# Kernel tuning notes

Measured on AMD Instinct MI355X. Metric: run time of the kernel, lower is better.

The kernel has to match this reference:

```python
import jax, jax.numpy as jnp
import numpy as np

IN_DIM = 256
LN_EPS = 1e-05


def _xavier(key, shape):
    fan_in, fan_out = shape[1], shape[0]
    a = np.sqrt(6.0 / (fan_in + fan_out)).astype(np.float32)
    return jax.random.uniform(key, shape, jnp.float32, -a, a)


def setup_inputs() -> dict:
    key = jax.random.key(0)
    ks = jax.random.split(key, 4)
    B, C, H, W = 32, IN_DIM, 32, 32
    x = jax.random.normal(ks[0], (B, C, H, W), jnp.float32)
    y = jax.random.normal(ks[1], (B, C, H, W), jnp.float32)
    # nn.MultiheadAttention in_proj: rows [0:C] -> Wq, [C:2C] -> Wk (V/out_proj
    # never influence the returned attention weights, so omitted).
    Wq = _xavier(ks[2], (C, C))
    Wk = _xavier(ks[3], (C, C))
    bq = jnp.zeros((C,), jnp.float32)
    bk = jnp.zeros((C,), jnp.float32)
    # norm1 LayerNorm affine params (norm2 is unused in forward).
    gamma = jnp.ones((C,), jnp.float32)
    beta = jnp.zeros((C,), jnp.float32)
    return {"x": x, "y": y, "gamma": gamma, "beta": beta,
            "Wq": Wq, "Wk": Wk, "bq": bq, "bk": bk}


def _layernorm(t, gamma, beta):
    mu = jnp.mean(t, axis=-1, keepdims=True)
    var = jnp.mean(jnp.square(t - mu), axis=-1, keepdims=True)
    return (t - mu) * jax.lax.rsqrt(var + LN_EPS) * gamma + beta


def reference(x, y, gamma, beta, Wq, Wk, bq, bk):
    B, C = x.shape[0], x.shape[1]
    # [B,C,H,W] -> [B, N, C]
    xs = x.reshape(B, C, -1).transpose(0, 2, 1)
    ys = y.reshape(B, C, -1).transpose(0, 2, 1)
    q = _layernorm(xs, gamma, beta) @ Wq.T + bq   # [B,N,C]
    k = _layernorm(ys, gamma, beta) @ Wk.T + bk   # [B,N,C]
    scale = 1.0 / np.sqrt(C).astype(np.float32)   # single head: head_dim = C
    scores = jnp.einsum('bnc,bmc->bnm', q, k) * scale  # [B,N,N]
    w = jax.nn.softmax(scores, axis=-1)
    # module returns weight.diagonal(dim1=1, dim2=2) -> [B, N]
    return jnp.diagonal(w, axis1=1, axis2=2)
```

## Files before the change

### kernel.cpp

```cpp
#include <hip/hip_runtime.h>
#include <math.h>

#define BATCH 32
#define CDIM  256
#define NDIM  1024
#define BN    (BATCH * NDIM)
#define BNC   ((size_t)BATCH * NDIM * CDIM)
#define LN_EPSF 1e-5f
#define SCALE 0.0625f

typedef __attribute__((ext_vector_type(8))) __bf16 bf16x8;
typedef __attribute__((ext_vector_type(4))) float f32x4;
typedef __attribute__((ext_vector_type(4))) unsigned short ushort4v;

static __device__ __forceinline__ unsigned short f2bf(float f) {
  unsigned u = __float_as_uint(f);
  unsigned r = (u + 0x7FFFu + ((u >> 16) & 1u)) >> 16;
  return (unsigned short)r;
}
static __device__ __forceinline__ float bf2f(unsigned short h) {
  return __uint_as_float(((unsigned)h) << 16);
}
static __device__ __forceinline__ void gload16(const void* g, void* l) {
  __builtin_amdgcn_global_load_lds((const __attribute__((address_space(1))) void*)g,
                                   (__attribute__((address_space(3))) void*)l, 16, 0, 0);
}


__global__ __launch_bounds__(256) void wsplit_k(const float* __restrict__ Wq,
                                                const float* __restrict__ Wk,
                                                unsigned short* __restrict__ wp) {
  int idx = blockIdx.x * 256 + threadIdx.x;
  float vq = Wq[idx];
  unsigned short hq = f2bf(vq);
  wp[idx] = hq;
  wp[65536 + idx] = f2bf(vq - bf2f(hq));
  float vk = Wk[idx];
  unsigned short hk = f2bf(vk);
  wp[131072 + idx] = hk;
  wp[196608 + idx] = f2bf(vk - bf2f(hk));
}

__global__ __launch_bounds__(256) void proj_k(const float* __restrict__ x,
                                              const float* __restrict__ y,
                                              const float* __restrict__ gamma,
                                              const float* __restrict__ beta,
                                              const float* __restrict__ bq,
                                              const float* __restrict__ bk,
                                              const unsigned short* __restrict__ wp,
                                              unsigned short* __restrict__ planes) {
  __shared__ unsigned short Lh[64][264];
  __shared__ unsigned short Ll[64][264];
  __shared__ float psum[16][64], psq[16][64];
  __shared__ float mu[64], ri[64], gl[CDIM], bl[CDIM], bias_s[CDIM];

  const int t = threadIdx.x;
  const int bz = blockIdx.y;
  const int b = bz >> 1, which = bz & 1;
  const int n0 = blockIdx.x * 64;
  const float* src = which ? y : x;

  gl[t] = gamma[t];
  bl[t] = beta[t];
  bias_s[t] = (which ? bk : bq)[t];

  const int nq = (t & 15) * 4;
  const int cs = (t >> 4) * 16;
  float4 xr[16];
#pragma unroll
  for (int i = 0; i < 16; ++i)
    xr[i] = *(const float4*)(src + ((size_t)b * CDIM + cs + i) * NDIM + n0 + nq);

  {
    float s[4] = {0.f, 0.f, 0.f, 0.f}, q[4] = {0.f, 0.f, 0.f, 0.f};
#pragma unroll
    for (int i = 0; i < 16; ++i) {
      float v0 = xr[i].x, v1 = xr[i].y, v2 = xr[i].z, v3 = xr[i].w;
      s[0] += v0; q[0] += v0 * v0;
      s[1] += v1; q[1] += v1 * v1;
      s[2] += v2; q[2] += v2 * v2;
      s[3] += v3; q[3] += v3 * v3;
    }
#pragma unroll
    for (int j = 0; j < 4; ++j) {
      psum[t >> 4][nq + j] = s[j];
      psq[t >> 4][nq + j] = q[j];
    }
  }
  __syncthreads();
  if (t < 64) {
    float S = 0.f, Q = 0.f;
#pragma unroll
    for (int s16 = 0; s16 < 16; ++s16) { S += psum[s16][t]; Q += psq[s16][t]; }
    float m = S * (1.f / CDIM);
    mu[t] = m;
    ri[t] = rsqrtf(fmaxf(Q * (1.f / CDIM) - m * m, 0.f) + LN_EPSF);
  }
  __syncthreads();

  {
    float mj[4], rj[4];
#pragma unroll
    for (int j = 0; j < 4; ++j) { mj[j] = mu[nq + j]; rj[j] = ri[nq + j]; }
#pragma unroll
    for (int k = 0; k < 8; ++k) {
      const int c0 = cs + 2 * k, c1 = c0 + 1;
      const float g0 = gl[c0], b0 = bl[c0], g1 = gl[c1], b1 = bl[c1];
      const float u0[4] = {xr[2 * k].x, xr[2 * k].y, xr[2 * k].z, xr[2 * k].w};
      const float u1[4] = {xr[2 * k + 1].x, xr[2 * k + 1].y, xr[2 * k + 1].z, xr[2 * k + 1].w};
#pragma unroll
      for (int j = 0; j < 4; ++j) {
        float v0 = (u0[j] - mj[j]) * rj[j] * g0 + b0;
        float v1 = (u1[j] - mj[j]) * rj[j] * g1 + b1;
        unsigned short h0 = f2bf(v0), h1 = f2bf(v1);
        unsigned short e0 = f2bf(v0 - bf2f(h0)), e1 = f2bf(v1 - bf2f(h1));
        *(unsigned*)&Lh[nq + j][c0] = ((unsigned)h1 << 16) | h0;
        *(unsigned*)&Ll[nq + j][c0] = ((unsigned)e1 << 16) | e0;
      }
    }
  }
  __syncthreads();

  const int w = t >> 6, l = t & 63;
  const int l15 = l & 15, l4 = l >> 4;
  const int co_base = w * 64;
  const unsigned short* Wh = wp + (size_t)which * 131072;
  const unsigned short* Wl = Wh + 65536;

  f32x4 acc[4][4];
#pragma unroll
  for (int i = 0; i < 4; ++i)
#pragma unroll
    for (int j = 0; j < 4; ++j) acc[i][j] = (f32x4){0.f, 0.f, 0.f, 0.f};

#pragma unroll
  for (int kt = 0; kt < 8; ++kt) {
    const int c0 = kt * 32;
    bf16x8 Ah[4], Al[4], Bh[4], Bl[4];
#pragma unroll
    for (int i = 0; i < 4; ++i) {
      size_t off = (size_t)(co_base + i * 16 + l15) * CDIM + c0 + l4 * 8;
      Ah[i] = *(const bf16x8*)(Wh + off);
      Al[i] = *(const bf16x8*)(Wl + off);
    }
#pragma unroll
    for (int j = 0; j < 4; ++j) {
      Bh[j] = *(const bf16x8*)&Lh[j * 16 + l15][c0 + l4 * 8];
      Bl[j] = *(const bf16x8*)&Ll[j * 16 + l15][c0 + l4 * 8];
    }
#pragma unroll
    for (int i = 0; i < 4; ++i)
#pragma unroll
      for (int j = 0; j < 4; ++j) {
        acc[i][j] = __builtin_amdgcn_mfma_f32_16x16x32_bf16(Ah[i], Bh[j], acc[i][j], 0, 0, 0);
        acc[i][j] = __builtin_amdgcn_mfma_f32_16x16x32_bf16(Ah[i], Bl[j], acc[i][j], 0, 0, 0);
        acc[i][j] = __builtin_amdgcn_mfma_f32_16x16x32_bf16(Al[i], Bh[j], acc[i][j], 0, 0, 0);
      }
  }

  unsigned short* ph = planes + (size_t)which * (2 * BNC);
  unsigned short* pl = ph + BNC;
#pragma unroll
  for (int i = 0; i < 4; ++i) {
    const int co4 = co_base + i * 16 + l4 * 4;
    float bias4[4];
#pragma unroll
    for (int r = 0; r < 4; ++r) bias4[r] = bias_s[co4 + r];
#pragma unroll
    for (int j = 0; j < 4; ++j) {
      size_t base = ((size_t)b * NDIM + n0 + j * 16 + l15) * CDIM + co4;
      ushort4v hs, ls;
#pragma unroll
      for (int r = 0; r < 4; ++r) {
        float v = acc[i][j][r] + bias4[r];
        unsigned short h = f2bf(v);
        hs[r] = h;
        ls[r] = f2bf(v - bf2f(h));
      }
      *(ushort4v*)(ph + base) = hs;
      *(ushort4v*)(pl + base) = ls;
    }
  }
}

__global__ __launch_bounds__(256) void attn_k(const unsigned short* __restrict__ planes,
                                              float* __restrict__ outp) {
  const unsigned short* qh = planes;
  const unsigned short* ql = planes + BNC;
  __shared__ unsigned short kbuf[2][2][8192];

  const int p = blockIdx.x;
  const int b = (p & 7) * 4 + ((p >> 3) & 3);
  const int n0 = (p >> 5) * 64;
  const int t = threadIdx.x;
  const int wid = t >> 6;
  const int l = t & 63;
  const int l15 = l & 15, l4 = l >> 4;

  bf16x8 ah[8], al[8];
  {
    size_t rowbase = ((size_t)b * NDIM + n0 + wid * 16 + l15) * CDIM + l4 * 8;
#pragma unroll
    for (int kt = 0; kt < 8; ++kt) {
      ah[kt] = *(const bf16x8*)(qh + rowbase + kt * 32);
      al[kt] = *(const bf16x8*)(ql + rowbase + kt * 32);
    }
  }

  const unsigned short* kb = planes + 2 * BNC + (size_t)b * NDIM * CDIM;
  const unsigned short* lb = planes + 3 * BNC + (size_t)b * NDIM * CDIM;

  auto stage = [&](int buf, int tt) {
    const int smt = tt >> 2, sk = tt & 3;
#pragma unroll
    for (int ii = 0; ii < 4; ++ii) {
      const int chunk = wid * 4 + ii;
      const int f = chunk & 7, s = chunk >> 3;
      size_t g = (size_t)(smt * 128 + f * 16 + l15) * CDIM + sk * 64 + s * 32 + l4 * 8;
      gload16(kb + g, &kbuf[buf][0][chunk * 512]);
      gload16(lb + g, &kbuf[buf][1][chunk * 512]);
    }
  };

  float M[4], S[4], dval[4];
#pragma unroll
  for (int r = 0; r < 4; ++r) { M[r] = -1e30f; S[r] = 0.f; dval[r] = 0.f; }

  stage(0, 0);
  __syncthreads();
  int cur = 0;

  for (int mt = 0; mt < 8; ++mt) {
    f32x4 acc[8];
#pragma unroll
    for (int f = 0; f < 8; ++f) acc[f] = (f32x4){0.f, 0.f, 0.f, 0.f};

    for (int kt64 = 0; kt64 < 4; ++kt64) {
      const int tt = mt * 4 + kt64;
      if (tt + 1 < 32) stage(cur ^ 1, tt + 1);
      const unsigned short* bhp = &kbuf[cur][0][0];
      const unsigned short* blp = &kbuf[cur][1][0];
#pragma unroll
      for (int s = 0; s < 2; ++s) {
        const int kq = kt64 * 2 + s;
#pragma unroll
        for (int f = 0; f < 8; ++f) {
          bf16x8 Bh = *(const bf16x8*)(bhp + (s * 8 + f) * 512 + l * 8);
          bf16x8 Bl = *(const bf16x8*)(blp + (s * 8 + f) * 512 + l * 8);
          acc[f] = __builtin_amdgcn_mfma_f32_16x16x32_bf16(ah[kq], Bh, acc[f], 0, 0, 0);
          acc[f] = __builtin_amdgcn_mfma_f32_16x16x32_bf16(ah[kq], Bl, acc[f], 0, 0, 0);
          acc[f] = __builtin_amdgcn_mfma_f32_16x16x32_bf16(al[kq], Bh, acc[f], 0, 0, 0);
        }
      }
      __syncthreads();
      cur ^= 1;
    }

    const int nrow = n0 + wid * 16 + l4 * 4;
#pragma unroll
    for (int r = 0; r < 4; ++r) {
      const int n = nrow + r;
      float tm = -1e30f;
#pragma unroll
      for (int f = 0; f < 8; ++f) tm = fmaxf(tm, acc[f][r]);
      tm *= SCALE;
#pragma unroll
      for (int off = 8; off >= 1; off >>= 1) tm = fmaxf(tm, __shfl_xor(tm, off));
      const float Mn = fmaxf(M[r], tm);
      float ps = 0.f;
#pragma unroll
      for (int f = 0; f < 8; ++f) ps += __expf(acc[f][r] * SCALE - Mn);
#pragma unroll
      for (int off = 8; off >= 1; off >>= 1) ps += __shfl_xor(ps, off);
      S[r] = S[r] * __expf(M[r] - Mn) + ps;
      M[r] = Mn;
#pragma unroll
      for (int f = 0; f < 8; ++f)
        if (mt * 128 + f * 16 + l15 == n) dval[r] = acc[f][r] * SCALE;
    }
  }

#pragma unroll
  for (int r = 0; r < 4; ++r) {
    const int n = n0 + wid * 16 + l4 * 4 + r;
    if ((n & 15) == l15)
      outp[(size_t)b * NDIM + n] = __expf(dval[r] - M[r]) / S[r];
  }
}

extern "C" void kernel_launch(void* const* d_in, const int* in_sizes, int n_in,
                              void* d_out, int out_size, void* d_ws, size_t ws_size,
                              hipStream_t stream) {
  (void)in_sizes; (void)n_in; (void)out_size; (void)ws_size;
  const float* x     = (const float*)d_in[0];
  const float* y     = (const float*)d_in[1];
  const float* gamma = (const float*)d_in[2];
  const float* beta  = (const float*)d_in[3];
  const float* Wq    = (const float*)d_in[4];
  const float* Wk    = (const float*)d_in[5];
  const float* bq    = (const float*)d_in[6];
  const float* bk    = (const float*)d_in[7];
  float* out = (float*)d_out;

  unsigned short* wp = (unsigned short*)d_ws;
  unsigned short* planes = wp + 262144;

  wsplit_k<<<256, 256, 0, stream>>>(Wq, Wk, wp);

  dim3 g2(NDIM / 64, BATCH * 2);
  proj_k<<<g2, 256, 0, stream>>>(x, y, gamma, beta, bq, bk, wp, planes);

  attn_k<<<512, 256, 0, stream>>>(planes, out);
}
```

Baseline: 223.1 us.

## Retile attention kernel to 2 waves with 32 query rows each and 64-key tiles

The attention kernel changes from 4 waves (16 query rows each, 128-key tiles) to 2 waves per block that each own 32 query rows across two row fragments, streaming 64-key tiles. Each B fragment loaded from LDS is now reused by two row fragments, which halves LDS reads per MFMA and halves the LDS staging buffer. The cost is more registers per thread (two sets of Q hi/lo fragments), fewer waves per block, and twice as many sync/stage iterations, which may reduce latency hiding.

```diff
diff --git a/kernel.cpp b/kernel.cpp
--- a/kernel.cpp
+++ b/kernel.cpp
@@ -183,27 +183,28 @@
   }
 }
 
-__global__ __launch_bounds__(256) void attn_k(const unsigned short* __restrict__ planes,
-                                              float* __restrict__ outp) {
+__global__ __launch_bounds__(128, 2) void attn_k(const unsigned short* __restrict__ planes,
+                                                 float* __restrict__ outp) {
   const unsigned short* qh = planes;
   const unsigned short* ql = planes + BNC;
-  __shared__ unsigned short kbuf[2][2][8192];
+  __shared__ unsigned short kbuf[2][8192];
 
   const int p = blockIdx.x;
   const int b = (p & 7) * 4 + ((p >> 3) & 3);
   const int n0 = (p >> 5) * 64;
   const int t = threadIdx.x;
-  const int wid = t >> 6;
+  const int w = t >> 6;
   const int l = t & 63;
   const int l15 = l & 15, l4 = l >> 4;
 
-  bf16x8 ah[8], al[8];
-  {
-    size_t rowbase = ((size_t)b * NDIM + n0 + wid * 16 + l15) * CDIM + l4 * 8;
-#pragma unroll
-    for (int kt = 0; kt < 8; ++kt) {
-      ah[kt] = *(const bf16x8*)(qh + rowbase + kt * 32);
-      al[kt] = *(const bf16x8*)(ql + rowbase + kt * 32);
+  bf16x8 ah[2][8], al[2][8];
+#pragma unroll
+  for (int rf = 0; rf < 2; ++rf) {
+    size_t rowbase = ((size_t)b * NDIM + n0 + w * 32 + rf * 16 + l15) * CDIM + l4 * 8;
+#pragma unroll
+    for (int kq = 0; kq < 8; ++kq) {
+      ah[rf][kq] = *(const bf16x8*)(qh + rowbase + kq * 32);
+      al[rf][kq] = *(const bf16x8*)(ql + rowbase + kq * 32);
     }
   }
 
@@ -211,81 +212,89 @@
   const unsigned short* lb = planes + 3 * BNC + (size_t)b * NDIM * CDIM;
 
   auto stage = [&](int buf, int tt) {
-    const int smt = tt >> 2, sk = tt & 3;
-#pragma unroll
-    for (int ii = 0; ii < 4; ++ii) {
-      const int chunk = wid * 4 + ii;
-      const int f = chunk & 7, s = chunk >> 3;
-      size_t g = (size_t)(smt * 128 + f * 16 + l15) * CDIM + sk * 64 + s * 32 + l4 * 8;
-      gload16(kb + g, &kbuf[buf][0][chunk * 512]);
-      gload16(lb + g, &kbuf[buf][1][chunk * 512]);
+    const int mt = tt >> 2, kc = tt & 3;
+#pragma unroll
+    for (int ii = 0; ii < 8; ++ii) {
+      const int chunk = w * 8 + ii;
+      const int cf = chunk & 3, kf = (chunk >> 2) & 1, pl = chunk >> 3;
+      size_t g = (size_t)(mt * 64 + cf * 16 + l15) * CDIM + kc * 64 + kf * 32 + l4 * 8;
+      gload16((pl ? lb : kb) + g, &kbuf[buf][chunk * 512]);
     }
   };
 
-  float M[4], S[4], dval[4];
-#pragma unroll
-  for (int r = 0; r < 4; ++r) { M[r] = -1e30f; S[r] = 0.f; dval[r] = 0.f; }
+  float M[8], S[8], dval[8];
+#pragma unroll
+  for (int i = 0; i < 8; ++i) { M[i] = -1e30f; S[i] = 0.f; dval[i] = 0.f; }
 
   stage(0, 0);
   __syncthreads();
   int cur = 0;
 
-  for (int mt = 0; mt < 8; ++mt) {
-    f32x4 acc[8];
-#pragma unroll
-    for (int f = 0; f < 8; ++f) acc[f] = (f32x4){0.f, 0.f, 0.f, 0.f};
-
-    for (int kt64 = 0; kt64 < 4; ++kt64) {
-      const int tt = mt * 4 + kt64;
-      if (tt + 1 < 32) stage(cur ^ 1, tt + 1);
-      const unsigned short* bhp = &kbuf[cur][0][0];
-      const unsigned short* blp = &kbuf[cur][1][0];
-#pragma unroll
-      for (int s = 0; s < 2; ++s) {
-        const int kq = kt64 * 2 + s;
-#pragma unroll
-        for (int f = 0; f < 8; ++f) {
-          bf16x8 Bh = *(const bf16x8*)(bhp + (s * 8 + f) * 512 + l * 8);
-          bf16x8 Bl = *(const bf16x8*)(blp + (s * 8 + f) * 512 + l * 8);
-          acc[f] = __builtin_amdgcn_mfma_f32_16x16x32_bf16(ah[kq], Bh, acc[f], 0, 0, 0);
-          acc[f] = __builtin_amdgcn_mfma_f32_16x16x32_bf16(ah[kq], Bl, acc[f], 0, 0, 0);
-          acc[f] = __builtin_amdgcn_mfma_f32_16x16x32_bf16(al[kq], Bh, acc[f], 0, 0, 0);
+  for (int mt = 0; mt < 16; ++mt) {
+    f32x4 acc[2][4];
+#pragma unroll
+    for (int rf = 0; rf < 2; ++rf)
+#pragma unroll
+      for (int cf = 0; cf < 4; ++cf) acc[rf][cf] = (f32x4){0.f, 0.f, 0.f, 0.f};
+
+    for (int kc = 0; kc < 4; ++kc) {
+      const int tt = mt * 4 + kc;
+      if (tt + 1 < 64) stage(cur ^ 1, tt + 1);
+#pragma unroll
+      for (int kf = 0; kf < 2; ++kf) {
+        const int kq = kc * 2 + kf;
+#pragma unroll
+        for (int cf = 0; cf < 4; ++cf) {
+          bf16x8 Bh = *(const bf16x8*)&kbuf[cur][(kf * 4 + cf) * 512 + l * 8];
+          bf16x8 Bl = *(const bf16x8*)&kbuf[cur][((2 + kf) * 4 + cf) * 512 + l * 8];
+#pragma unroll
+          for (int rf = 0; rf < 2; ++rf) {
+            acc[rf][cf] = __builtin_amdgcn_mfma_f32_16x16x32_bf16(ah[rf][kq], Bh, acc[rf][cf], 0, 0, 0);
+            acc[rf][cf] = __builtin_amdgcn_mfma_f32_16x16x32_bf16(ah[rf][kq], Bl, acc[rf][cf], 0, 0, 0);
+            acc[rf][cf] = __builtin_amdgcn_mfma_f32_16x16x32_bf16(al[rf][kq], Bh, acc[rf][cf], 0, 0, 0);
+          }
         }
       }
       __syncthreads();
       cur ^= 1;
     }
 
-    const int nrow = n0 + wid * 16 + l4 * 4;
+#pragma unroll
+    for (int rf = 0; rf < 2; ++rf) {
+#pragma unroll
+      for (int r = 0; r < 4; ++r) {
+        const int idx = rf * 4 + r;
+        const int n = n0 + w * 32 + rf * 16 + l4 * 4 + r;
+        float tm = -1e30f;
+#pragma unroll
+        for (int cf = 0; cf < 4; ++cf) tm = fmaxf(tm, acc[rf][cf][r]);
+        tm *= SCALE;
+#pragma unroll
+        for (int off = 8; off >= 1; off >>= 1) tm = fmaxf(tm, __shfl_xor(tm, off));
+        const float Mn = fmaxf(M[idx], tm);
+        float ps = 0.f;
+#pragma unroll
+        for (int cf = 0; cf < 4; ++cf) ps += __expf(acc[rf][cf][r] * SCALE - Mn);
+#pragma unroll
+        for (int off = 8; off >= 1; off >>= 1) ps += __shfl_xor(ps, off);
+        S[idx] = S[idx] * __expf(M[idx] - Mn) + ps;
+        M[idx] = Mn;
+#pragma unroll
+        for (int cf = 0; cf < 4; ++cf)
+          if (mt * 64 + cf * 16 + l15 == n) dval[idx] = acc[rf][cf][r] * SCALE;
+      }
+    }
+  }
+
+#pragma unroll
+  for (int rf = 0; rf < 2; ++rf)
 #pragma unroll
     for (int r = 0; r < 4; ++r) {
-      const int n = nrow + r;
-      float tm = -1e30f;
-#pragma unroll
-      for (int f = 0; f < 8; ++f) tm = fmaxf(tm, acc[f][r]);
-      tm *= SCALE;
-#pragma unroll
-      for (int off = 8; off >= 1; off >>= 1) tm = fmaxf(tm, __shfl_xor(tm, off));
-      const float Mn = fmaxf(M[r], tm);
-      float ps = 0.f;
-#pragma unroll
-      for (int f = 0; f < 8; ++f) ps += __expf(acc[f][r] * SCALE - Mn);
-#pragma unroll
-      for (int off = 8; off >= 1; off >>= 1) ps += __shfl_xor(ps, off);
-      S[r] = S[r] * __expf(M[r] - Mn) + ps;
-      M[r] = Mn;
-#pragma unroll
-      for (int f = 0; f < 8; ++f)
-        if (mt * 128 + f * 16 + l15 == n) dval[r] = acc[f][r] * SCALE;
-    }
-  }
-
-#pragma unroll
-  for (int r = 0; r < 4; ++r) {
-    const int n = n0 + wid * 16 + l4 * 4 + r;
-    if ((n & 15) == l15)
-      outp[(size_t)b * NDIM + n] = __expf(dval[r] - M[r]) / S[r];
-  }
+      const int idx = rf * 4 + r;
+      const int n = n0 + w * 32 + rf * 16 + l4 * 4 + r;
+      if (l15 == l4 * 4 + r)
+        outp[(size_t)b * NDIM + n] = __expf(dval[idx] - M[idx]) / S[idx];
+    }
 }
 
 extern "C" void kernel_launch(void* const* d_in, const int* in_sizes, int n_in,
@@ -310,5 +319,5 @@
   dim3 g2(NDIM / 64, BATCH * 2);
   proj_k<<<g2, 256, 0, stream>>>(x, y, gamma, beta, bq, bk, wp, planes);
 
-  attn_k<<<512, 256, 0, stream>>>(planes, out);
-}
+  attn_k<<<512, 128, 0, stream>>>(planes, out);
+}
```

Result: slower. 250.4 us (+12.2%).
